# Performance work log

Measured on AMD Instinct MI355X. Metric: run time of the kernel, lower is better.

Reference implementation:

```python
import jax, jax.numpy as jnp
import numpy as np

N = 5  # patch_neighbors
DIL = 1

def _grid_sample(img, grid):
    """Bilinear grid_sample, padding_mode='border', align_corners=False.
    img: [B,C,H,W]; grid: [B,Hg,Wg,2] in [-1,1] (x,y). Returns [B,C,Hg,Wg]."""
    B, C, H, W = img.shape
    gx, gy = grid[..., 0], grid[..., 1]
    ix = ((gx + 1.0) * W - 1.0) * 0.5
    iy = ((gy + 1.0) * H - 1.0) * 0.5
    x0 = jnp.floor(ix); y0 = jnp.floor(iy)
    wx = (ix - x0)[:, None]; wy = (iy - y0)[:, None]  # [B,1,Hg,Wg]
    x0c = jnp.clip(x0, 0, W - 1).astype(jnp.int32)
    x1c = jnp.clip(x0 + 1, 0, W - 1).astype(jnp.int32)
    y0c = jnp.clip(y0, 0, H - 1).astype(jnp.int32)
    y1c = jnp.clip(y0 + 1, 0, H - 1).astype(jnp.int32)
    gather = jax.vmap(lambda im, yi, xi: im[:, yi, xi])
    v00 = gather(img, y0c, x0c); v01 = gather(img, y0c, x1c)
    v10 = gather(img, y1c, x0c); v11 = gather(img, y1c, x1c)
    return (v00 * (1 - wx) * (1 - wy) + v01 * wx * (1 - wy)
            + v10 * (1 - wx) * wy + v11 * wx * wy)

def _make_patch_grid(B, H, W, dilation=DIL):
    # offsets unpacked as (oy, ox) in the original code (note duplicated (d,0))
    offsets = [(dilation, 0), (0, -dilation), (0, 0), (0, dilation), (dilation, 0)]
    ys, xs = jnp.meshgrid(jnp.arange(H, dtype=jnp.float32),
                          jnp.arange(W, dtype=jnp.float32), indexing='ij')
    parts = []
    for oy, ox in offsets:
        xn = (xs + ox) / ((W - 1) / 2.0) - 1.0
        yn = (ys + oy) / ((H - 1) / 2.0) - 1.0
        parts.append(jnp.stack([xn, yn], axis=-1))  # [H,W,2]
    g = jnp.concatenate(parts, axis=0)  # [N*H, W, 2]
    return jnp.broadcast_to(g, (B,) + g.shape)

def setup_inputs():
    key = jax.random.key(0)
    ks = jax.random.split(key, 10)
    B, C, D, H, W = 2, 32, 8, 512, 512
    ref_feature = jax.random.normal(ks[0], (B, C, H, W), jnp.float32)
    n = jax.random.normal(ks[1], (B, 3, H, W), jnp.float32)
    normal = n / (jnp.linalg.norm(n, axis=1, keepdims=True) + 1e-8)
    depth_values = jax.random.uniform(ks[2], (B, D, H, W), jnp.float32) * 500.0 + 425.0
    intri = jnp.broadcast_to(jnp.array([[float(W), 0.0, W / 2.0],
                                        [0.0, float(W), H / 2.0],
                                        [0.0, 0.0, 1.0]], jnp.float32), (B, 3, 3))
    w0 = jax.random.normal(ks[3], (16, 1), jnp.float32) * 0.5
    s0 = jax.random.uniform(ks[4], (16,), jnp.float32) + 0.5
    b0 = jax.random.normal(ks[5], (16,), jnp.float32) * 0.1
    w1 = jax.random.normal(ks[6], (8, 16), jnp.float32) * 0.25
    s1 = jax.random.uniform(ks[7], (8,), jnp.float32) + 0.5
    b1 = jax.random.normal(ks[8], (8,), jnp.float32) * 0.1
    w2 = jax.random.normal(ks[9], (1, 8), jnp.float32) * 0.35
    b2 = jnp.zeros((1,), jnp.float32)
    return {"ref_feature": ref_feature, "normal": normal, "depth_values": depth_values,
            "intri": intri, "w0": w0, "s0": s0, "b0": b0, "w1": w1, "s1": s1,
            "b1": b1, "w2": w2, "b2": b2}

def _conv1x1(x, w):  # x: [B,I,D,H,W], w: [O,I]
    return jnp.einsum('oi,bidhw->bodhw', w, x)

def reference(ref_feature, normal, depth_values, intri, w0, s0, b0, w1, s1, b1, w2, b2):
    B, C, H, W = ref_feature.shape
    D = depth_values.shape[1]
    grid = _make_patch_grid(B, H, W)  # [B, N*H, W, 2]

    # ---- get_detph_shift ----
    ys, xs = jnp.meshgrid(jnp.arange(H, dtype=jnp.float32),
                          jnp.arange(W, dtype=jnp.float32), indexing='ij')
    xy = jnp.broadcast_to(jnp.stack([xs, ys])[None], (B, 2, H, W))
    xy_s = _grid_sample(xy, grid).reshape(B, 2, N, H, W)
    fx, fy = intri[:, 0, 0], intri[:, 1, 1]
    cx, cy = intri[:, 0, 2], intri[:, 1, 2]
    r = lambda v: v[:, None, None, None]
    u = (xy_s[:, 0] - r(cx)) / r(fx)  # [B,N,H,W]
    v = (xy_s[:, 1] - r(cy)) / r(fy)
    nx, ny, nz = normal[:, 0:1], normal[:, 1:2], normal[:, 2:3]  # [B,1,H,W]
    c = N // 2
    num = nx * u[:, c:c + 1] + ny * v[:, c:c + 1] + nz     # [B,1,H,W]
    den = nx * u + ny * v + nz                              # [B,N,H,W]
    den = jnp.where(jnp.abs(den) < 1e-8, jnp.sign(den) * 1e-8, den)
    den = jnp.where(jnp.abs(den) < 1e-8, 1e-8, den)
    w = num / den
    w = jnp.where(jnp.isnan(w) | jnp.isinf(w), 1.0, w)
    # faithful to torch .view(B, N, -1, H, W) on a [B,D,N,H,W] tensor (flat reinterpret)
    depth_shift = (w[:, None] * depth_values[:, :, None]).reshape(B, N, D, H, W)

    # ---- get_patch_similarity (sim='cos' on normals) ----
    ns = _grid_sample(normal, grid).reshape(B, 3, N, H, W)
    dot = jnp.sum(ns * normal[:, :, None], axis=1)
    na = jnp.sqrt(jnp.sum(ns * ns, axis=1))
    nb = jnp.sqrt(jnp.sum(normal * normal, axis=1))[:, None]
    sim = dot / (jnp.maximum(na, 1e-8) * jnp.maximum(nb, 1e-8))
    sim = sim / jnp.sum(sim, axis=1, keepdims=True)  # [B,N,H,W]

    # ---- patch-gathered, similarity-weighted ref feature ----
    rpf = _grid_sample(ref_feature, grid).reshape(B, C, N, H, W) * sim[:, None]

    # ---- similarity volume (neighbor-sum, channel-mean contraction) ----
    sim_vol = jnp.einsum('bcnhw,bndhw->bdhw', rpf, depth_shift) / C  # [B,D,H,W]

    # ---- PixelwiseNet (1x1 Conv3d + BN(folded) + ReLU stack) ----
    x1 = sim_vol[:, None]  # [B,1,D,H,W]
    e = lambda p: p[None, :, None, None, None]
    h = jax.nn.relu(_conv1x1(x1, w0) * e(s0) + e(b0))
    h = jax.nn.relu(_conv1x1(h, w1) * e(s1) + e(b1))
    logits = _conv1x1(h, w2) + e(b2)
    vw = jax.nn.sigmoid(logits[:, 0])                 # [B,D,H,W]
    view_weight = jnp.max(vw, axis=1, keepdims=True)  # [B,1,H,W]

    return sim_vol * view_weight  # [B,D,H,W]
```

## Files before the change

### kernel.cpp

```cpp
#include <hip/hip_runtime.h>
#include <math.h>

#define HW 262144
#define TAB_SPARSE_OFF 8193
#define FSUM_OFF 32768

__device__ __forceinline__ int clip511f(float t) { return (int)fminf(fmaxf(t, 0.0f), 511.0f); }

__device__ float mlp_lg(float t,
                        const float* __restrict__ w0, const float* __restrict__ s0,
                        const float* __restrict__ b0, const float* __restrict__ w1,
                        const float* __restrict__ s1, const float* __restrict__ b1,
                        const float* __restrict__ w2, const float* __restrict__ b2) {
    float h0[16];
    #pragma unroll
    for (int k = 0; k < 16; ++k)
        h0[k] = fmaxf((w0[k] * t) * s0[k] + b0[k], 0.0f);
    float lg = b2[0];
    #pragma unroll
    for (int j = 0; j < 8; ++j) {
        float a1 = 0.0f;
        #pragma unroll
        for (int k = 0; k < 16; ++k) a1 += w1[j * 16 + k] * h0[k];
        float h1 = fmaxf(a1 * s1[j] + b1[j], 0.0f);
        lg += w2[j] * h1;
    }
    return lg;
}

__global__ __launch_bounds__(256) void tab_kernel(
    const float* __restrict__ w0, const float* __restrict__ s0, const float* __restrict__ b0,
    const float* __restrict__ w1, const float* __restrict__ s1, const float* __restrict__ b1,
    const float* __restrict__ w2, const float* __restrict__ b2,
    float* __restrict__ ws) {
    int i = blockIdx.x * 256 + threadIdx.x;
    if (i <= 8192) {
        float t = -1024.0f + 0.25f * (float)i;
        ws[i] = mlp_lg(t, w0, s0, b0, w1, s1, b1, w2, b2);
    }
    int j = i - 8448;
    if (j >= 0 && j <= 8192) {
        float t = -131072.0f + 32.0f * (float)j;
        ws[TAB_SPARSE_OFF + j] = mlp_lg(t, w0, s0, b0, w1, s1, b1, w2, b2);
    }
}

__global__ __launch_bounds__(256) void fsum_kernel(const float* __restrict__ rf,
                                                   float* __restrict__ fsum) {
    int t = blockIdx.x * 256 + threadIdx.x;
    int b = t >> 16;
    int q = t & 65535;
    const float4* src = reinterpret_cast<const float4*>(rf) + (size_t)(b * 32) * 65536 + q;
    float4 acc = make_float4(0.f, 0.f, 0.f, 0.f);
    #pragma unroll
    for (int c = 0; c < 32; ++c) {
        float4 v = src[(size_t)c * 65536];
        acc.x += v.x; acc.y += v.y; acc.z += v.z; acc.w += v.w;
    }
    reinterpret_cast<float4*>(fsum)[t] = acc;
}

struct Axis { float wx, om; int c0, c1; };
__device__ __forceinline__ Axis axis_eval(int t_int) {
#pragma clang fp contract(off)
    const float RCP = (float)(1.0 / 255.5);
    float q = (float)t_int * RCP;
    float gp = (q - 1.0f) + 1.0f;
    float ix = ((gp * 512.0f) - 1.0f) * 0.5f;
    float x0 = floorf(ix);
    Axis a;
    a.wx = ix - x0;
    a.om = 1.0f - a.wx;
    a.c0 = clip511f(x0);
    a.c1 = clip511f(x0 + 1.0f);
    return a;
}

__global__ __launch_bounds__(256) void patch_kernel(
    const float* __restrict__ nrm, const float* __restrict__ dv,
    const float* __restrict__ intri, const float* __restrict__ ws,
    const float* __restrict__ w0, const float* __restrict__ s0, const float* __restrict__ b0,
    const float* __restrict__ w1, const float* __restrict__ s1, const float* __restrict__ b1,
    const float* __restrict__ w2, const float* __restrict__ b2,
    float* __restrict__ out)
{
    __shared__ float sW[201];
    int tid = threadIdx.x;
    if (tid < 201) {
        float vv;
        if      (tid < 16)  vv = w0[tid];
        else if (tid < 32)  vv = s0[tid - 16];
        else if (tid < 48)  vv = b0[tid - 32];
        else if (tid < 176) vv = w1[tid - 48];
        else if (tid < 184) vv = s1[tid - 176];
        else if (tid < 192) vv = b1[tid - 184];
        else if (tid < 200) vv = w2[tid - 192];
        else                vv = b2[0];
        sW[tid] = vv;
    }
    __syncthreads();

    int pid = blockIdx.x * 256 + tid;
    int b = pid >> 18;
    int r = pid & (HW - 1);
    int y = r >> 9;
    int x = r & 511;

    float fx = intri[b * 9 + 0], cx = intri[b * 9 + 2];
    float fy = intri[b * 9 + 4], cy = intri[b * 9 + 5];

    const float* nb = nrm + (size_t)(b * 3) * HW;
    const float* fb = ws + FSUM_OFF + (size_t)b * HW;

    Axis axm = axis_eval(x - 1);
    Axis ax0 = axis_eval(x);
    Axis axp = axis_eval(x + 1);
    Axis ay0 = axis_eval(y);
    Axis ayp = axis_eval(y + 1);

    float wxt[4]  = { ax0.wx, axm.wx, ax0.wx, axp.wx };
    float omxt[4] = { ax0.om, axm.om, ax0.om, axp.om };
    float wyt[4]  = { ayp.wx, ay0.wx, ay0.wx, ay0.wx };
    float omyt[4] = { ayp.om, ay0.om, ay0.om, ay0.om };
    int xc0[4] = { ax0.c0, axm.c0, ax0.c0, axp.c0 };
    int xc1[4] = { ax0.c1, axm.c1, ax0.c1, axp.c1 };
    int yc0[4] = { ayp.c0, ay0.c0, ay0.c0, ay0.c0 };
    int yc1[4] = { ayp.c1, ay0.c1, ay0.c1, ay0.c1 };

    int i00[4], i01[4], i10[4], i11[4];
    #pragma unroll
    for (int n = 0; n < 4; ++n) {
        i00[n] = yc0[n] * 512 + xc0[n]; i01[n] = yc0[n] * 512 + xc1[n];
        i10[n] = yc1[n] * 512 + xc0[n]; i11[n] = yc1[n] * 512 + xc1[n];
    }

    float gx_[4][4], gy_[4][4], gz_[4][4], gF_[4][4];
    #pragma unroll
    for (int n = 0; n < 4; ++n) {
        gx_[n][0] = nb[i00[n]];        gx_[n][1] = nb[i01[n]];
        gx_[n][2] = nb[i10[n]];        gx_[n][3] = nb[i11[n]];
        gy_[n][0] = nb[HW + i00[n]];   gy_[n][1] = nb[HW + i01[n]];
        gy_[n][2] = nb[HW + i10[n]];   gy_[n][3] = nb[HW + i11[n]];
        gz_[n][0] = nb[2*HW + i00[n]]; gz_[n][1] = nb[2*HW + i01[n]];
        gz_[n][2] = nb[2*HW + i10[n]]; gz_[n][3] = nb[2*HW + i11[n]];
        gF_[n][0] = fb[i00[n]];        gF_[n][1] = fb[i01[n]];
        gF_[n][2] = fb[i10[n]];        gF_[n][3] = fb[i11[n]];
    }
    float nx = nb[r], ny = nb[HW + r], nz = nb[2 * HW + r];
    size_t dvbase = (size_t)(b * 8) * HW + (size_t)r;
    float dvv[8];
    #pragma unroll
    for (int d = 0; d < 8; ++d) dvv[d] = dv[dvbase + (size_t)d * HW];

    float sim[5], F[5], ss, wv[5];
    {
#pragma clang fp contract(off)
        float u[5], v[5];
        float nbn = sqrtf((nx * nx + ny * ny) + nz * nz);

        for (int n = 0; n < 4; ++n) {
            float wxf = wxt[n], omx = omxt[n], wyf = wyt[n], omy = omyt[n];
            int x0 = xc0[n], x1 = xc1[n], y0 = yc0[n], y1 = yc1[n];

            {
                float m00 = (float)x0 * omx, m01 = (float)x1 * wxf;
                float m10 = (float)x0 * omx, m11 = (float)x1 * wxf;
                float A = m00 * omy, B = m01 * omy, C = m10 * wyf, D = m11 * wyf;
                float xs_ = ((A + B) + C) + D;
                float n00 = (float)y0 * omx, n01 = (float)y0 * wxf;
                float n10 = (float)y1 * omx, n11 = (float)y1 * wxf;
                float A2 = n00 * omy, B2 = n01 * omy, C2 = n10 * wyf, D2 = n11 * wyf;
                float ys_ = ((A2 + B2) + C2) + D2;
                u[n] = (xs_ - cx) / fx;
                v[n] = (ys_ - cy) / fy;
            }

            float nsx, nsy, nsz;
            {
                float m00 = gx_[n][0] * omx, m01 = gx_[n][1] * wxf;
                float m10 = gx_[n][2] * omx, m11 = gx_[n][3] * wxf;
                nsx = ((m00 * omy + m01 * omy) + m10 * wyf) + m11 * wyf;
                float p00 = gy_[n][0] * omx, p01 = gy_[n][1] * wxf;
                float p10 = gy_[n][2] * omx, p11 = gy_[n][3] * wxf;
                nsy = ((p00 * omy + p01 * omy) + p10 * wyf) + p11 * wyf;
                float q00 = gz_[n][0] * omx, q01 = gz_[n][1] * wxf;
                float q10 = gz_[n][2] * omx, q11 = gz_[n][3] * wxf;
                nsz = ((q00 * omy + q01 * omy) + q10 * wyf) + q11 * wyf;
            }

            float dot = (nsx * nx + nsy * ny) + nsz * nz;
            float na  = sqrtf((nsx * nsx + nsy * nsy) + nsz * nsz);
            sim[n] = dot / (fmaxf(na, 1e-8f) * fmaxf(nbn, 1e-8f));

            float m00 = gF_[n][0] * omx, m01 = gF_[n][1] * wxf;
            float m10 = gF_[n][2] * omx, m11 = gF_[n][3] * wxf;
            F[n] = ((m00 * omy + m01 * omy) + m10 * wyf) + m11 * wyf;
        }
        u[4] = u[0]; v[4] = v[0]; sim[4] = sim[0]; F[4] = F[0];

        ss = ((sim[0] + sim[1]) + (sim[2] + sim[3])) + sim[4];

        float num = (nx * u[2] + ny * v[2]) + nz;
        for (int n = 0; n < 5; ++n) {
            float den = (nx * u[n] + ny * v[n]) + nz;
            if (fabsf(den) < 1e-8f) den = (den < 0.0f) ? -1e-8f : 1e-8f;
            float w_ = num * __builtin_amdgcn_rcpf(den);
            if (!isfinite(w_)) w_ = 1.0f;
            wv[n] = w_;
        }
    }

    float rss = __builtin_amdgcn_rcpf(ss);
    float qv[5];
    #pragma unroll
    for (int n = 0; n < 5; ++n) qv[n] = (sim[n] * rss) * F[n];

    float sv[8];
    #pragma unroll
    for (int dp = 0; dp < 8; ++dp) {
        float acc = 0.0f;
        #pragma unroll
        for (int n = 0; n < 5; ++n) {
            const int flat = n * 8 + dp;
            acc += qv[n] * (wv[flat % 5] * dvv[flat / 5]);
        }
        sv[dp] = acc * 0.03125f;
    }

    float mx = -1e30f;
    #pragma unroll
    for (int d = 0; d < 8; ++d) {
        float t = sv[d];
        float at = fabsf(t);
        float lg;
        if (at < 131072.0f) {
            bool dense = at < 1024.0f;
            const float* g = dense ? ws : (ws + TAB_SPARSE_OFF);
            float T0  = dense ? -1024.0f : -131072.0f;
            float inv = dense ? 4.0f : 0.03125f;
            float p = (t - T0) * inv;
            int idx = (int)p;
            float fr = p - (float)idx;
            float g0 = g[idx], g1 = g[idx + 1];
            lg = g0 + fr * (g1 - g0);
        } else {
            float h0[16];
            #pragma unroll
            for (int k = 0; k < 16; ++k)
                h0[k] = fmaxf((sW[k] * t) * sW[16 + k] + sW[32 + k], 0.0f);
            lg = sW[200];
            #pragma unroll
            for (int j = 0; j < 8; ++j) {
                float a1 = 0.0f;
                #pragma unroll
                for (int k = 0; k < 16; ++k) a1 += sW[48 + j * 16 + k] * h0[k];
                float h1 = fmaxf(a1 * sW[176 + j] + sW[184 + j], 0.0f);
                lg += sW[192 + j] * h1;
            }
        }
        mx = fmaxf(mx, lg);
    }
    float vw = 1.0f / (1.0f + expf(-mx));

    #pragma unroll
    for (int d = 0; d < 8; ++d)
        out[dvbase + (size_t)d * HW] = sv[d] * vw;
}

extern "C" void kernel_launch(void* const* d_in, const int* in_sizes, int n_in,
                              void* d_out, int out_size, void* d_ws, size_t ws_size,
                              hipStream_t stream) {
    const float* rf    = (const float*)d_in[0];
    const float* nrm   = (const float*)d_in[1];
    const float* dv    = (const float*)d_in[2];
    const float* intri = (const float*)d_in[3];
    const float* w0    = (const float*)d_in[4];
    const float* s0    = (const float*)d_in[5];
    const float* b0    = (const float*)d_in[6];
    const float* w1    = (const float*)d_in[7];
    const float* s1    = (const float*)d_in[8];
    const float* b1    = (const float*)d_in[9];
    const float* w2    = (const float*)d_in[10];
    const float* b2    = (const float*)d_in[11];
    float* out = (float*)d_out;
    float* ws  = (float*)d_ws;

    tab_kernel<<<66, 256, 0, stream>>>(w0, s0, b0, w1, s1, b1, w2, b2, ws);
    fsum_kernel<<<512, 256, 0, stream>>>(rf, ws + FSUM_OFF);
    patch_kernel<<<2048, 256, 0, stream>>>(nrm, dv, intri, ws,
                                           w0, s0, b0, w1, s1, b1, w2, b2, out);
}
```

Baseline: 48.06 us.

## Stage normal and feature-sum halo tiles in shared memory for bilinear gathers

Each block now covers a half row of 256 pixels and first loads a 4-row by 260-column halo tile of the three normal channels and the feature sum into LDS. The 64 scattered global gathers per thread become LDS reads at precomputed tile offsets, and the block-to-pixel mapping is rewritten to match. This is meant to cut redundant global and L2 traffic from overlapping neighbour reads. The cost is about 17KB of LDS per block, which may limit occupancy, plus an extra cooperative load and barrier before any compute starts.

```diff
diff --git a/kernel.cpp b/kernel.cpp
--- a/kernel.cpp
+++ b/kernel.cpp
@@ -4,6 +4,7 @@
 #define HW 262144
 #define TAB_SPARSE_OFF 8193
 #define FSUM_OFF 32768
+#define TW 260
 
 __device__ __forceinline__ int clip511f(float t) { return (int)fminf(fmaxf(t, 0.0f), 511.0f); }
 
@@ -84,8 +85,21 @@
     const float* __restrict__ w2, const float* __restrict__ b2,
     float* __restrict__ out)
 {
+    __shared__ float tile[4 * 4 * TW];
     __shared__ float sW[201];
+
     int tid = threadIdx.x;
+    int bid = blockIdx.x;
+    int b = bid >> 10;
+    int rowblk = bid & 1023;
+    int y = rowblk >> 1;
+    int bx = (rowblk & 1) << 8;
+    int x = bx + tid;
+    int r = y * 512 + x;
+
+    int ry_base = y - 1;
+    int cx_base = bx - 2;
+
     if (tid < 201) {
         float vv;
         if      (tid < 16)  vv = w0[tid];
@@ -98,19 +112,24 @@
         else                vv = b2[0];
         sW[tid] = vv;
     }
+
+    const float* fsum_b = ws + FSUM_OFF + (size_t)b * HW;
+    const float* nrm_b  = nrm + (size_t)(b * 3) * HW;
+    for (int idx = tid; idx < 4 * 4 * TW; idx += 256) {
+        int ch  = idx / (4 * TW);
+        int rem = idx - ch * 4 * TW;
+        int row = rem / TW;
+        int col = rem - row * TW;
+        int ir = min(max(ry_base + row, 0), 511);
+        int ic = min(max(cx_base + col, 0), 511);
+        float vsrc = (ch < 3) ? nrm_b[(size_t)ch * HW + ir * 512 + ic]
+                              : fsum_b[ir * 512 + ic];
+        tile[idx] = vsrc;
+    }
     __syncthreads();
-
-    int pid = blockIdx.x * 256 + tid;
-    int b = pid >> 18;
-    int r = pid & (HW - 1);
-    int y = r >> 9;
-    int x = r & 511;
 
     float fx = intri[b * 9 + 0], cx = intri[b * 9 + 2];
     float fy = intri[b * 9 + 4], cy = intri[b * 9 + 5];
-
-    const float* nb = nrm + (size_t)(b * 3) * HW;
-    const float* fb = ws + FSUM_OFF + (size_t)b * HW;
 
     Axis axm = axis_eval(x - 1);
     Axis ax0 = axis_eval(x);
@@ -127,26 +146,20 @@
     int yc0[4] = { ayp.c0, ay0.c0, ay0.c0, ay0.c0 };
     int yc1[4] = { ayp.c1, ay0.c1, ay0.c1, ay0.c1 };
 
-    int i00[4], i01[4], i10[4], i11[4];
+    int o00[4], o01[4], o10[4], o11[4];
     #pragma unroll
     for (int n = 0; n < 4; ++n) {
-        i00[n] = yc0[n] * 512 + xc0[n]; i01[n] = yc0[n] * 512 + xc1[n];
-        i10[n] = yc1[n] * 512 + xc0[n]; i11[n] = yc1[n] * 512 + xc1[n];
-    }
-
-    float gx_[4][4], gy_[4][4], gz_[4][4], gF_[4][4];
-    #pragma unroll
-    for (int n = 0; n < 4; ++n) {
-        gx_[n][0] = nb[i00[n]];        gx_[n][1] = nb[i01[n]];
-        gx_[n][2] = nb[i10[n]];        gx_[n][3] = nb[i11[n]];
-        gy_[n][0] = nb[HW + i00[n]];   gy_[n][1] = nb[HW + i01[n]];
-        gy_[n][2] = nb[HW + i10[n]];   gy_[n][3] = nb[HW + i11[n]];
-        gz_[n][0] = nb[2*HW + i00[n]]; gz_[n][1] = nb[2*HW + i01[n]];
-        gz_[n][2] = nb[2*HW + i10[n]]; gz_[n][3] = nb[2*HW + i11[n]];
-        gF_[n][0] = fb[i00[n]];        gF_[n][1] = fb[i01[n]];
-        gF_[n][2] = fb[i10[n]];        gF_[n][3] = fb[i11[n]];
-    }
-    float nx = nb[r], ny = nb[HW + r], nz = nb[2 * HW + r];
+        int tc0 = xc0[n] - cx_base, tc1 = xc1[n] - cx_base;
+        int tr0 = yc0[n] - ry_base, tr1 = yc1[n] - ry_base;
+        o00[n] = tr0 * TW + tc0; o01[n] = tr0 * TW + tc1;
+        o10[n] = tr1 * TW + tc0; o11[n] = tr1 * TW + tc1;
+    }
+
+    int ctr = 1 * TW + (tid + 2);
+    float nx = tile[ctr];
+    float ny = tile[4 * TW + ctr];
+    float nz = tile[8 * TW + ctr];
+
     size_t dvbase = (size_t)(b * 8) * HW + (size_t)r;
     float dvv[8];
     #pragma unroll
@@ -177,14 +190,14 @@
 
             float nsx, nsy, nsz;
             {
-                float m00 = gx_[n][0] * omx, m01 = gx_[n][1] * wxf;
-                float m10 = gx_[n][2] * omx, m11 = gx_[n][3] * wxf;
+                float m00 = tile[o00[n]] * omx, m01 = tile[o01[n]] * wxf;
+                float m10 = tile[o10[n]] * omx, m11 = tile[o11[n]] * wxf;
                 nsx = ((m00 * omy + m01 * omy) + m10 * wyf) + m11 * wyf;
-                float p00 = gy_[n][0] * omx, p01 = gy_[n][1] * wxf;
-                float p10 = gy_[n][2] * omx, p11 = gy_[n][3] * wxf;
+                float p00 = tile[4*TW + o00[n]] * omx, p01 = tile[4*TW + o01[n]] * wxf;
+                float p10 = tile[4*TW + o10[n]] * omx, p11 = tile[4*TW + o11[n]] * wxf;
                 nsy = ((p00 * omy + p01 * omy) + p10 * wyf) + p11 * wyf;
-                float q00 = gz_[n][0] * omx, q01 = gz_[n][1] * wxf;
-                float q10 = gz_[n][2] * omx, q11 = gz_[n][3] * wxf;
+                float q00 = tile[8*TW + o00[n]] * omx, q01 = tile[8*TW + o01[n]] * wxf;
+                float q10 = tile[8*TW + o10[n]] * omx, q11 = tile[8*TW + o11[n]] * wxf;
                 nsz = ((q00 * omy + q01 * omy) + q10 * wyf) + q11 * wyf;
             }
 
@@ -192,8 +205,8 @@
             float na  = sqrtf((nsx * nsx + nsy * nsy) + nsz * nsz);
             sim[n] = dot / (fmaxf(na, 1e-8f) * fmaxf(nbn, 1e-8f));
 
-            float m00 = gF_[n][0] * omx, m01 = gF_[n][1] * wxf;
-            float m10 = gF_[n][2] * omx, m11 = gF_[n][3] * wxf;
+            float m00 = tile[12*TW + o00[n]] * omx, m01 = tile[12*TW + o01[n]] * wxf;
+            float m10 = tile[12*TW + o10[n]] * omx, m11 = tile[12*TW + o11[n]] * wxf;
             F[n] = ((m00 * omy + m01 * omy) + m10 * wyf) + m11 * wyf;
         }
         u[4] = u[0]; v[4] = v[0]; sim[4] = sim[0]; F[4] = F[0];
```

New measurement: 52.97 us. +10.2%, slower.
